# Performance work log

Measured on AMD Instinct MI355X. Metric: run time of the kernel, lower is better.

The kernel has to match this reference:

```python
import jax, jax.numpy as jnp
import numpy as np

K_TOP = 2
NUM_HEADS = 8
NOISE_EPS = 0.01
GATE_EPS = 1e-9
LOSS_COEF = 0.01


def _xavier(key, shape):
    fan_in, fan_out = shape[-2], shape[-1]
    lim = float(np.sqrt(6.0 / (fan_in + fan_out)))
    return jax.random.uniform(key, shape, jnp.float32, -lim, lim)


def setup_inputs():
    key = jax.random.key(0)
    ks = jax.random.split(key, 12)
    B, S, D, E = 32, 512, 512, 8
    return {
        "q": jax.random.normal(ks[0], (B, S, D), jnp.float32),
        "k": jax.random.normal(ks[1], (B, S, D), jnp.float32),
        "v": jax.random.normal(ks[2], (B, S, D), jnp.float32),
        "mask": jnp.ones((1, 1, S, S), jnp.int32),
        "w_gate": _xavier(ks[3], (D, E)),
        "w_noise": _xavier(ks[4], (D, E)),
        "Wq": _xavier(ks[5], (E, D, D)),
        "bq": jnp.zeros((E, D), jnp.float32),
        "Wk": _xavier(ks[6], (E, D, D)),
        "bk": jnp.zeros((E, D), jnp.float32),
        "Wv": _xavier(ks[7], (E, D, D)),
        "bv": jnp.zeros((E, D), jnp.float32),
        "Wo": _xavier(ks[8], (E, D, D)),
        "bo": jnp.zeros((E, D), jnp.float32),
    }


def _cv_squared(x):
    # torch .var() is unbiased (ddof=1)
    return jnp.var(x, ddof=1) / (jnp.mean(x) ** 2 + 1e-10)


def _moe_attention(q, k, v, mask, w_gate, w_noise, Wq, bq, Wk, bk, Wv, bv, Wo, bo):
    B, S, D = q.shape
    E = w_gate.shape[1]
    H = NUM_HEADS
    dh = D // H

    # x[x != x] = 0 (in-place nan scrub of q, used for gating AND as query)
    qc = jnp.where(jnp.isnan(q), jnp.zeros((), q.dtype), q)

    # noisy top-k gating; the python loop sum_i x[:,i,:] @ W == x.sum(1) @ W
    xs = qc.sum(axis=1)                                  # [B, D]
    clean_logits = xs @ w_gate                           # [B, E]
    raw_noise = xs @ w_noise
    noise_std = jax.nn.softplus(raw_noise) + NOISE_EPS   # train=True
    noise = jax.random.normal(jax.random.key(42), clean_logits.shape, clean_logits.dtype)
    noisy_logits = clean_logits + noise * noise_std

    top_logits, top_idx = jax.lax.top_k(noisy_logits, K_TOP + 1)  # [B, k+1]
    tk_logits = top_logits[:, :K_TOP]
    tk_idx = top_idx[:, :K_TOP]                          # [B, k]
    tk_gates = jax.nn.softmax(tk_logits, axis=1) + GATE_EPS
    gates = jnp.zeros((B, E), clean_logits.dtype).at[jnp.arange(B)[:, None], tk_idx].set(tk_gates)

    # load via prob-in-top-k (noisy_gating and k < num_experts)
    thr_in = top_logits[:, K_TOP][:, None]
    thr_out = top_logits[:, K_TOP - 1][:, None]
    is_in = noisy_logits > thr_in
    cdf = jax.scipy.stats.norm.cdf
    prob = jnp.where(is_in, cdf((clean_logits - thr_in) / noise_std),
                     cdf((clean_logits - thr_out) / noise_std))
    load = prob.sum(axis=0)
    importance = gates.sum(axis=0)
    loss = (_cv_squared(importance) + _cv_squared(load)) * LOSS_COEF

    # sparse dispatch == per (batch, slot) run the selected expert's MHA.
    # Gather expert weights per selected slot: [B, k, D, D].
    def proj(x, W, b):
        return jnp.einsum('bsd,bjdf->bjsf', x, W[tk_idx]) + b[tk_idx][:, :, None, :]

    Q = proj(qc, Wq, bq).reshape(B, K_TOP, S, H, dh)
    Kx = proj(k, Wk, bk).reshape(B, K_TOP, S, H, dh)
    V = proj(v, Wv, bv).reshape(B, K_TOP, S, H, dh)

    scale = jnp.asarray(1.0 / np.sqrt(dh), q.dtype)
    scores = jnp.einsum('bjqhd,bjkhd->bjhqk', Q, Kx) * scale   # [B,k,H,S,S]
    m = mask[:, None]                                          # [1,1,1,S,S]
    scores = jnp.where(m == 0, jnp.asarray(-1e9, scores.dtype), scores)
    attn = jax.nn.softmax(scores, axis=-1)
    ctx = jnp.einsum('bjhqk,bjkhd->bjqhd', attn, V).reshape(B, K_TOP, S, D)
    out_e = jnp.einsum('bjsd,bjdf->bjsf', ctx, Wo[tk_idx]) + bo[tk_idx][:, :, None, :]

    # combine: sum_j gate * exp(out), clamp zeros to eps, log
    combined = jnp.einsum('bj,bjsd->bsd', tk_gates, jnp.exp(out_e))
    eps = jnp.asarray(np.finfo(np.float64).eps, combined.dtype)
    combined = jnp.where(combined == 0, eps, combined)
    return jnp.log(combined), loss


def reference(q, k, v, mask, w_gate, w_noise, Wq, bq, Wk, bk, Wv, bv, Wo, bo):
    return _moe_attention(q, k, v, mask, w_gate, w_noise, Wq, bq, Wk, bk, Wv, bv, Wo, bo)
```

## Files before the change

### kernel.cpp

```cpp
#include <hip/hip_runtime.h>
#include <math.h>

typedef unsigned int u32;
typedef unsigned long long u64;
typedef unsigned short u16t;

#define SD   512
#define EE   8
#define DH   64
#define SDSQ (512*512)
#define LDSW 72

typedef __attribute__((ext_vector_type(8))) short bfrag8;
typedef __attribute__((ext_vector_type(4))) float f32x4;
typedef __attribute__((ext_vector_type(8))) unsigned short u16x8;

typedef const __attribute__((address_space(1))) void gas_void;
typedef __attribute__((address_space(3))) void las_void;

#define MFMA_B16(a,b,c) __builtin_amdgcn_mfma_f32_16x16x32_bf16((a),(b),(c),0,0,0)

__device__ __forceinline__ u32 rotl32(u32 x, int r){ return (x<<r)|(x>>(32-r)); }

__device__ __forceinline__ u16t bf_hi(float a){
  u32 x; __builtin_memcpy(&x,&a,4);
  u32 r = x + 0x7fffu + ((x>>16)&1u);
  return (u16t)(r>>16);
}
__device__ __forceinline__ float bf_f(u16t h){
  u32 x = ((u32)h)<<16; float f; __builtin_memcpy(&f,&x,4); return f;
}
__device__ __forceinline__ void split2(float a, u16t& h, u16t& l){
  h = bf_hi(a);
  l = bf_hi(a - bf_f(h));
}

__device__ __forceinline__ void gload16(const u16t* g, u16t* l){
  __builtin_amdgcn_global_load_lds((gas_void*)g, (las_void*)l, 16, 0, 0);
}

__device__ __forceinline__ void threefry_0_42(u32 x0, u32 x1, u32& o0, u32& o1){
  const u32 k0=0u, k1=42u;
  const u32 ks2 = k0 ^ k1 ^ 0x1BD11BDAu;
  const int R0[4]={13,15,26,6}, R1[4]={17,29,16,24};
  x0 += k0; x1 += k1;
  #pragma unroll
  for(int r=0;r<4;r++){ x0+=x1; x1=rotl32(x1,R0[r]); x1^=x0; }
  x0+=k1; x1+=ks2+1u;
  #pragma unroll
  for(int r=0;r<4;r++){ x0+=x1; x1=rotl32(x1,R1[r]); x1^=x0; }
  x0+=ks2; x1+=k0+2u;
  #pragma unroll
  for(int r=0;r<4;r++){ x0+=x1; x1=rotl32(x1,R0[r]); x1^=x0; }
  x0+=k0; x1+=k1+3u;
  #pragma unroll
  for(int r=0;r<4;r++){ x0+=x1; x1=rotl32(x1,R1[r]); x1^=x0; }
  x0+=k1; x1+=ks2+4u;
  #pragma unroll
  for(int r=0;r<4;r++){ x0+=x1; x1=rotl32(x1,R0[r]); x1^=x0; }
  x0+=ks2; x1+=k0+5u;
  o0 = x0; o1 = x1;
}

__device__ double erfinv64(double x){
  double w = -log((1.0 - x) * (1.0 + x));
  double p;
  if (w < 5.0){
    w = w - 2.5;
    p = 2.81022636e-08;
    p = 3.43273939e-07 + p*w;
    p = -3.5233877e-06 + p*w;
    p = -4.39150654e-06 + p*w;
    p = 0.00021858087  + p*w;
    p = -0.00125372503 + p*w;
    p = -0.00417768164 + p*w;
    p = 0.246640727    + p*w;
    p = 1.50140941     + p*w;
  } else {
    w = sqrt(w) - 3.0;
    p = -0.000200214257;
    p = 0.000100950558 + p*w;
    p = 0.00134934322  + p*w;
    p = -0.00367342844 + p*w;
    p = 0.00573950773  + p*w;
    p = -0.0076224613  + p*w;
    p = 0.00943887047  + p*w;
    p = 1.00167406     + p*w;
    p = 2.83297682     + p*w;
  }
  double r = p * x;
  #pragma unroll
  for (int it=0; it<2; ++it){
    double e = erf(r) - x;
    r -= e / (1.1283791670955126 * exp(-r*r));
  }
  return r;
}

__device__ double jax_noise_part32(int i){
  u32 o0, o1;
  threefry_0_42(0u, (u32)i, o0, o1);
  u32 bits = o0 ^ o1;
  u32 fb = (bits >> 9) | 0x3f800000u;
  float f; __builtin_memcpy(&f, &fb, 4);
  f -= 1.0f;
  u32 lob = 0xBF7FFFFFu;
  float lo; __builtin_memcpy(&lo, &lob, 4);
  float t = f * 2.0f;
  float u = t + lo;
  u = fmaxf(u, lo);
  return 1.4142135623730951 * erfinv64((double)u);
}

__global__ __launch_bounds__(256) void k_cvt_x(
  const float* __restrict__ src, u16t* __restrict__ dh, u16t* __restrict__ dl, int clean)
{
  const int n4 = 32*SDSQ/4;
  int i = blockIdx.x*256 + threadIdx.x;
  if (i >= n4) return;
  float4 r = ((const float4*)src)[i];
  float a[4] = {r.x, r.y, r.z, r.w};
  if (clean){
    #pragma unroll
    for (int u=0;u<4;u++) if (isnan(a[u])) a[u] = 0.f;
  }
  u16t h[4], l[4];
  #pragma unroll
  for (int u=0;u<4;u++) split2(a[u], h[u], l[u]);
  ((ushort4*)dh)[i] = make_ushort4(h[0],h[1],h[2],h[3]);
  ((ushort4*)dl)[i] = make_ushort4(l[0],l[1],l[2],l[3]);
}

__global__ __launch_bounds__(256) void k_cvt_w(
  const float* __restrict__ W, u16t* __restrict__ th, u16t* __restrict__ tl)
{
  __shared__ u16t Th[64*LDSW], Tl[64*LDSW];
  int e = blockIdx.z;
  int k0 = blockIdx.y*64, f0 = blockIdx.x*64;
  int tid = threadIdx.x;
  int r = tid>>2, c4 = (tid&3)*16;
  const float* Wp = W + (size_t)e*SDSQ + (size_t)(k0+r)*SD + f0 + c4;
  #pragma unroll
  for (int i=0;i<4;i++){
    float4 rv = *(const float4*)(Wp + 4*i);
    float a[4]={rv.x,rv.y,rv.z,rv.w};
    #pragma unroll
    for (int u=0;u<4;u++){
      u16t h,l; split2(a[u],h,l);
      Th[(c4+4*i+u)*LDSW + r] = h;
      Tl[(c4+4*i+u)*LDSW + r] = l;
    }
  }
  __syncthreads();
  u16t* dh = th + (size_t)e*SDSQ + (size_t)(f0+r)*SD + k0 + c4;
  u16t* dl = tl + (size_t)e*SDSQ + (size_t)(f0+r)*SD + k0 + c4;
  *(u16x8*)dh     = *(const u16x8*)&Th[r*LDSW + c4];
  *(u16x8*)(dh+8) = *(const u16x8*)&Th[r*LDSW + c4 + 8];
  *(u16x8*)dl     = *(const u16x8*)&Tl[r*LDSW + c4];
  *(u16x8*)(dl+8) = *(const u16x8*)&Tl[r*LDSW + c4 + 8];
}

__global__ void k_xs(const float* __restrict__ q, double* __restrict__ xs){
  int b = blockIdx.x, d = threadIdx.x;
  const float* p = q + (size_t)b*SDSQ + d;
  double acc = 0.0;
  for (int s=0; s<SD; ++s){
    float f = p[(size_t)s*SD];
    if (!isnan(f)) acc += (double)f;
  }
  xs[b*SD + d] = acc;
}

__global__ __launch_bounds__(256) void k_gate(
    const double* __restrict__ xs, const float* __restrict__ wg,
    const float* __restrict__ wn, int* __restrict__ tk_idx,
    float* __restrict__ tk_gates, float* __restrict__ out_loss)
{
  __shared__ double cl_s[256], sd_s[256], nz_s[256], pr_s[256];
  __shared__ double thrI_s[32], thrO_s[32], g0_s[32], g1_s[32];
  __shared__ int i0_s[32], i1_s[32];
  int tid = threadIdx.x;
  int b = tid >> 3, e = tid & 7;
  double c=0.0, n=0.0;
  const double* xr = xs + b*SD;
  for (int d=0; d<SD; ++d){
    double x = xr[d];
    c += x * (double)wg[d*EE + e];
    n += x * (double)wn[d*EE + e];
  }
  double sp = fmax(n, 0.0) + log1p(exp(-fabs(n)));
  double sdv = sp + 0.01;
  double nz = c + jax_noise_part32(tid) * sdv;
  cl_s[tid]=c; sd_s[tid]=sdv; nz_s[tid]=nz;
  __syncthreads();
  if (tid < 32){
    int bb = tid;
    double v0=-INFINITY,v1=-INFINITY,v2=-INFINITY; int i0=0,i1=0;
    for (int ee=0; ee<8; ++ee){
      double vv = nz_s[bb*8+ee];
      if (vv > v0){ v2=v1; v1=v0;i1=i0; v0=vv;i0=ee; }
      else if (vv > v1){ v2=v1; v1=vv;i1=ee; }
      else if (vv > v2){ v2=vv; }
    }
    double e1 = exp(v1 - v0);
    double s = 1.0 + e1;
    double g0 = 1.0/s + 1e-9, g1 = e1/s + 1e-9;
    tk_idx[bb*2+0]=i0; tk_idx[bb*2+1]=i1;
    tk_gates[bb*2+0]=(float)g0; tk_gates[bb*2+1]=(float)g1;
    i0_s[bb]=i0; i1_s[bb]=i1; g0_s[bb]=g0; g1_s[bb]=g1;
    thrI_s[bb]=v2; thrO_s[bb]=v1;
  }
  __syncthreads();
  {
    double thrI = thrI_s[b], thrO = thrO_s[b];
    bool isin = nz_s[tid] > thrI;
    double t = (cl_s[tid] - (isin ? thrI : thrO)) / sd_s[tid];
    pr_s[tid] = 0.5 * (1.0 + erf(t * 0.7071067811865476));
  }
  __syncthreads();
  if (tid == 0){
    double imp[8], ld[8];
    for (int i=0;i<8;i++){ imp[i]=0.0; ld[i]=0.0; }
    for (int bb=0; bb<32; ++bb){
      imp[i0_s[bb]] += g0_s[bb];
      imp[i1_s[bb]] += g1_s[bb];
    }
    for (int i=0;i<256;i++) ld[i&7] += pr_s[i];
    double loss = 0.0;
    for (int a=0;a<2;a++){
      double* arr = a ? ld : imp;
      double mu=0.0; for(int i=0;i<8;i++) mu += arr[i]; mu *= 0.125;
      double var=0.0; for(int i=0;i<8;i++){ double dd=arr[i]-mu; var += dd*dd; }
      var *= (1.0/7.0);
      loss += var / (mu*mu + 1e-10);
    }
    loss *= 0.01;
    out_loss[0] = (float)loss;
  }
}

__global__ __launch_bounds__(256) void k_proj(
  const u16t* __restrict__ qh, const u16t* __restrict__ ql,
  const u16t* __restrict__ kh, const u16t* __restrict__ kl,
  const u16t* __restrict__ vh, const u16t* __restrict__ vl,
  const u16t* __restrict__ wqh, const u16t* __restrict__ wql,
  const u16t* __restrict__ wkh, const u16t* __restrict__ wkl,
  const u16t* __restrict__ wvh, const u16t* __restrict__ wvl,
  const float* __restrict__ bq, const float* __restrict__ bk, const float* __restrict__ bv,
  const int* __restrict__ tk_idx, int pair0,
  u16t* __restrict__ Qh, u16t* __restrict__ Ql,
  u16t* __restrict__ Kh, u16t* __restrict__ Kl,
  u16t* __restrict__ Vth, u16t* __restrict__ Vtl)
{
  __shared__ __align__(16) u16t SM[4*128*64];
  int Nb = gridDim.x*gridDim.y*gridDim.z;
  int flat = blockIdx.x + gridDim.x*(blockIdx.y + gridDim.y*blockIdx.z);
  int nf = (flat & 7)*(Nb>>3) + (flat>>3);
  int bxx = nf & 3, byy = (nf>>2) & 3, z = nf >> 4;
  int lp = z/3, m = z - lp*3;
  int gp = pair0 + lp;
  int b = gp >> 1;
  int e = tk_idx[gp] & 7;
  const u16t *Xh, *Xl, *Wh, *Wl; const float* bias; u16t *Yh, *Yl;
  if (m==0){ Xh=qh; Xl=ql; Wh=wqh; Wl=wql; bias=bq; Yh=Qh;  Yl=Ql;  }
  else if (m==1){ Xh=kh; Xl=kl; Wh=wkh; Wl=wkl; bias=bk; Yh=Kh;  Yl=Kl;  }
  else { Xh=vh; Xl=vl; Wh=wvh; Wl=wvl; bias=bv; Yh=Vth; Yl=Vtl; }
  bool tr = (m==2);
  Xh += (size_t)b*SDSQ; Xl += (size_t)b*SDSQ;
  Wh += (size_t)e*SDSQ; Wl += (size_t)e*SDSQ;
  bias += e*SD;
  Yh += (size_t)lp*SDSQ; Yl += (size_t)lp*SDSQ;

  int tid = threadIdx.x, w = tid>>6, lane = tid&63;
  int q16 = lane&15, quad = lane>>4;
  int wm = w>>1, wnn = w&1;
  int s0 = byy*128, f0 = bxx*128;
  int row8 = lane>>3, cc = lane&7;
  int soff = (cc ^ row8)*8;
  int sw = q16 & 7;
  int aH_off = tr ? 16384 : 0;
  int bH_off = tr ? 0 : 16384;

  f32x4 acc[4][4];
  #pragma unroll
  for (int i=0;i<4;i++)
    #pragma unroll
    for (int j=0;j<4;j++) acc[i][j] = (f32x4){0.f,0.f,0.f,0.f};

  for (int k0=0;k0<SD;k0+=64){
    #pragma unroll
    for (int t=0;t<4;t++){
      int br = w*32 + t*8;
      int gr = br + row8;
      size_t ga  = (size_t)(s0+gr)*SD + k0 + soff;
      size_t gbo = (size_t)(f0+gr)*SD + k0 + soff;
      gload16(Xh + ga,  &SM[0     + br*64]);
      gload16(Xl + ga,  &SM[8192  + br*64]);
      gload16(Wh + gbo, &SM[16384 + br*64]);
      gload16(Wl + gbo, &SM[24576 + br*64]);
    }
    __syncthreads();
    #pragma unroll
    for (int kk=0;kk<2;kk++){
      int ch = kk*4 + quad;
      int co = (ch ^ sw)*8;
      bfrag8 fAH[4], fAL[4], fBH[4], fBL[4];
      #pragma unroll
      for (int i=0;i<4;i++){
        int ra = wm*64  + i*16 + q16;
        int rb = wnn*64 + i*16 + q16;
        fAH[i] = *(const bfrag8*)&SM[aH_off        + ra*64 + co];
        fAL[i] = *(const bfrag8*)&SM[aH_off + 8192 + ra*64 + co];
        fBH[i] = *(const bfrag8*)&SM[bH_off        + rb*64 + co];
        fBL[i] = *(const bfrag8*)&SM[bH_off + 8192 + rb*64 + co];
      }
      #pragma unroll
      for (int i=0;i<4;i++)
        #pragma unroll
        for (int j=0;j<4;j++){
          acc[i][j] = MFMA_B16(fAH[i], fBH[j], acc[i][j]);
          acc[i][j] = MFMA_B16(fAH[i], fBL[j], acc[i][j]);
          acc[i][j] = MFMA_B16(fAL[i], fBH[j], acc[i][j]);
        }
    }
    __syncthreads();
  }
  if (!tr){
    #pragma unroll
    for (int i=0;i<4;i++){
      #pragma unroll
      for (int j=0;j<4;j++){
        int f = f0 + wnn*64 + j*16 + q16;
        float bb = bias[f];
        #pragma unroll
        for (int rr=0;rr<4;rr++){
          int s = s0 + wm*64 + i*16 + quad*4 + rr;
          u16t hh, ll; split2(acc[i][j][rr] + bb, hh, ll);
          size_t o = (size_t)s*SD + f;
          Yh[o] = hh; Yl[o] = ll;
        }
      }
    }
  } else {
    #pragma unroll
    for (int i=0;i<4;i++){
      #pragma unroll
      for (int rr=0;rr<4;rr++){
        int fr = f0 + wm*64 + i*16 + quad*4 + rr;
        float bb = bias[fr];
        #pragma unroll
        for (int j=0;j<4;j++){
          int scol = s0 + wnn*64 + j*16 + q16;
          u16t hh, ll; split2(acc[i][j][rr] + bb, hh, ll);
          size_t o = (size_t)fr*SD + scol;
          Yh[o] = hh; Yl[o] = ll;
        }
      }
    }
  }
}

__global__ __launch_bounds__(256, 4) void k_attn(
  const u16t* __restrict__ Qh, const u16t* __restrict__ Ql,
  const u16t* __restrict__ Kh, const u16t* __restrict__ Kl,
  const u16t* __restrict__ Vth, const u16t* __restrict__ Vtl,
  u16t* __restrict__ Ch, u16t* __restrict__ Cl)
{
  __shared__ __align__(16) u16t SM[20480];
  int tid = threadIdx.x;
  int w = tid>>6, lane = tid&63, q16 = lane&15, quad = lane>>4;
  int Nb = gridDim.x*gridDim.y*gridDim.z;
  int flat = blockIdx.x + gridDim.x*(blockIdx.y + gridDim.y*blockIdx.z);
  int nf = (flat & 7)*(Nb>>3) + (flat>>3);
  int qt = nf & 7, h = (nf>>3) & 7, lp = nf >> 6;
  int s0 = qt*64;
  const size_t base  = (size_t)lp*SDSQ + h*DH;
  const size_t vbase = (size_t)lp*SDSQ + (size_t)h*DH*SD;
  int row8 = lane>>3, cc = lane&7;
  int soff = (cc ^ row8)*8;
  int sw = q16 & 7;

  bfrag8 qH[2], qL[2];
  {
    const u16t* qp  = Qh + base + (size_t)(s0 + w*16 + q16)*SD + quad*8;
    const u16t* qp2 = Ql + base + (size_t)(s0 + w*16 + q16)*SD + quad*8;
    qH[0] = *(const bfrag8*)(qp);
    qH[1] = *(const bfrag8*)(qp + 32);
    qL[0] = *(const bfrag8*)(qp2);
    qL[1] = *(const bfrag8*)(qp2 + 32);
  }

  float m_row[4], l_row[4];
  f32x4 ctx[4];
  #pragma unroll
  for (int rr=0;rr<4;rr++){ m_row[rr]=-INFINITY; l_row[rr]=0.f; }
  #pragma unroll
  for (int nt=0;nt<4;nt++) ctx[nt] = (f32x4){0.f,0.f,0.f,0.f};

  for (int kt=0; kt<8; ++kt){
    #pragma unroll
    for (int t=0;t<2;t++){
      int br = w*16 + t*8;
      int gr = br + row8;
      size_t gk = base + (size_t)(kt*64+gr)*SD + soff;
      gload16(Kh + gk, &SM[0    + br*64]);
      gload16(Kl + gk, &SM[4096 + br*64]);
      size_t gv = vbase + (size_t)gr*SD + kt*64 + soff;
      gload16(Vth + gv, &SM[8192  + br*64]);
      gload16(Vtl + gv, &SM[12288 + br*64]);
    }
    __syncthreads();

    f32x4 sc[4];
    #pragma unroll
    for (int nt=0;nt<4;nt++) sc[nt] = (f32x4){0.f,0.f,0.f,0.f};
    #pragma unroll
    for (int kk=0;kk<2;kk++){
      int co = ((kk*4+quad) ^ sw)*8;
      #pragma unroll
      for (int nt=0;nt<4;nt++){
        bfrag8 bH = *(const bfrag8*)&SM[0    + (nt*16+q16)*64 + co];
        bfrag8 bL = *(const bfrag8*)&SM[4096 + (nt*16+q16)*64 + co];
        sc[nt] = MFMA_B16(qH[kk],bH,sc[nt]);
        sc[nt] = MFMA_B16(qH[kk],bL,sc[nt]);
        sc[nt] = MFMA_B16(qL[kk],bH,sc[nt]);
      }
    }
    #pragma unroll
    for (int nt=0;nt<4;nt++)
      #pragma unroll
      for (int rr=0;rr<4;rr++) sc[nt][rr] *= 0.125f;

    float alpha[4];
    #pragma unroll
    for (int rr=0;rr<4;rr++){
      float mx = sc[0][rr];
      #pragma unroll
      for (int nt=1;nt<4;nt++) mx = fmaxf(mx, sc[nt][rr]);
      mx = fmaxf(mx, __shfl_xor(mx, 1));
      mx = fmaxf(mx, __shfl_xor(mx, 2));
      mx = fmaxf(mx, __shfl_xor(mx, 4));
      mx = fmaxf(mx, __shfl_xor(mx, 8));
      float nm = fmaxf(m_row[rr], mx);
      alpha[rr] = expf(m_row[rr] - nm);
      m_row[rr] = nm;
    }
    #pragma unroll
    for (int rr=0;rr<4;rr++){
      float S = 0.f;
      #pragma unroll
      for (int nt=0;nt<4;nt++){
        float p = expf(sc[nt][rr] - m_row[rr]);
        sc[nt][rr] = p;
        S += p;
      }
      S += __shfl_xor(S, 1);
      S += __shfl_xor(S, 2);
      S += __shfl_xor(S, 4);
      S += __shfl_xor(S, 8);
      l_row[rr] = l_row[rr]*alpha[rr] + S;
      #pragma unroll
      for (int nt=0;nt<4;nt++) ctx[nt][rr] *= alpha[rr];
    }
    #pragma unroll
    for (int nt=0;nt<4;nt++){
      int c = nt*2 + (q16>>3);
      #pragma unroll
      for (int rr=0;rr<4;rr++){
        int prow = quad*4 + rr;
        SM[16384 + (w*16+prow)*64 + ((c ^ (prow&7))*8) + (q16&7)] = bf_hi(sc[nt][rr]);
      }
    }

    #pragma unroll
    for (int kk2=0;kk2<2;kk2++){
      int co2 = ((kk2*4+quad) ^ sw)*8;
      bfrag8 aP = *(const bfrag8*)&SM[16384 + (w*16+q16)*64 + co2];
      #pragma unroll
      for (int nt=0;nt<4;nt++){
        bfrag8 vH = *(const bfrag8*)&SM[8192  + (nt*16+q16)*64 + co2];
        bfrag8 vL = *(const bfrag8*)&SM[12288 + (nt*16+q16)*64 + co2];
        ctx[nt] = MFMA_B16(aP,vH,ctx[nt]);
        ctx[nt] = MFMA_B16(aP,vL,ctx[nt]);
      }
    }
    __syncthreads();
  }
  #pragma unroll
  for (int rr=0;rr<4;rr++){
    float inv = 1.f / l_row[rr];
    #pragma unroll
    for (int nt=0;nt<4;nt++){
      int s = s0 + w*16 + quad*4 + rr;
      u16t hh, ll; split2(ctx[nt][rr]*inv, hh, ll);
      size_t o = base + (size_t)s*SD + nt*16 + q16;
      Ch[o] = hh; Cl[o] = ll;
    }
  }
}

__global__ __launch_bounds__(256) void k_out(
  const u16t* __restrict__ Ch, const u16t* __restrict__ Cl,
  const u16t* __restrict__ Wth, const u16t* __restrict__ Wtl,
  const float* __restrict__ bo, const int* __restrict__ tk_idx,
  const float* __restrict__ tk_gates, int pair0, float* __restrict__ out)
{
  __shared__ __align__(16) u16t Ah[64*64], Al[64*64];
  __shared__ __align__(16) u16t Bh[64*64], Bl[64*64];
  int Nb = gridDim.x*gridDim.y*gridDim.z;
  int flat = blockIdx.x + gridDim.x*(blockIdx.y + gridDim.y*blockIdx.z);
  int nf = (flat & 7)*(Nb>>3) + (flat>>3);
  int bxx = nf & 7, byy = (nf>>3) & 7, lb = nf >> 6;
  int gb = (pair0 >> 1) + lb;
  int tid = threadIdx.x;
  int w = tid>>6, lane = tid&63, q16 = lane&15, quad = lane>>4;
  int s0 = byy*64, f0 = bxx*64;
  int row8 = lane>>3, cc = lane&7;
  int soff = (cc ^ row8)*8;
  int sw = q16 & 7;

  f32x4 acc2[2][4];
  #pragma unroll
  for (int j=0;j<2;j++)
    #pragma unroll
    for (int nt=0;nt<4;nt++) acc2[j][nt] = (f32x4){0.f,0.f,0.f,0.f};

  for (int j=0;j<2;++j){
    int e = tk_idx[pair0 + lb*2 + j] & 7;
    const u16t* AH = Ch + (size_t)(lb*2+j)*SDSQ;
    const u16t* AL = Cl + (size_t)(lb*2+j)*SDSQ;
    const u16t* WH = Wth + (size_t)e*SDSQ;
    const u16t* WL = Wtl + (size_t)e*SDSQ;
    for (int k0=0;k0<SD;k0+=64){
      #pragma unroll
      for (int t=0;t<2;t++){
        int br = w*16 + t*8, gr = br + row8;
        size_t ga  = (size_t)(s0+gr)*SD + k0 + soff;
        size_t gbo = (size_t)(f0+gr)*SD + k0 + soff;
        gload16(AH + ga,  &Ah[br*64]);
        gload16(AL + ga,  &Al[br*64]);
        gload16(WH + gbo, &Bh[br*64]);
        gload16(WL + gbo, &Bl[br*64]);
      }
      __syncthreads();
      #pragma unroll
      for (int kk=0;kk<2;kk++){
        int co = ((kk*4+quad) ^ sw)*8;
        bfrag8 aH = *(const bfrag8*)&Ah[(w*16+q16)*64 + co];
        bfrag8 aL = *(const bfrag8*)&Al[(w*16+q16)*64 + co];
        #pragma unroll
        for (int nt=0;nt<4;nt++){
          bfrag8 bH = *(const bfrag8*)&Bh[(nt*16+q16)*64 + co];
          bfrag8 bL = *(const bfrag8*)&Bl[(nt*16+q16)*64 + co];
          acc2[j][nt] = MFMA_B16(aH,bH,acc2[j][nt]);
          acc2[j][nt] = MFMA_B16(aH,bL,acc2[j][nt]);
          acc2[j][nt] = MFMA_B16(aL,bH,acc2[j][nt]);
        }
      }
      __syncthreads();
    }
  }
  int e0 = tk_idx[pair0 + lb*2 + 0] & 7, e1 = tk_idx[pair0 + lb*2 + 1] & 7;
  float g0 = tk_gates[pair0 + lb*2 + 0], g1 = tk_gates[pair0 + lb*2 + 1];
  #pragma unroll
  for (int nt=0;nt<4;nt++){
    #pragma unroll
    for (int rr=0;rr<4;rr++){
      int s = s0 + w*16 + quad*4 + rr;
      int f = f0 + nt*16 + q16;
      float o0 = acc2[0][nt][rr] + bo[e0*SD+f];
      float o1 = acc2[1][nt][rr] + bo[e1*SD+f];
      float cmb = g0*expf(o0) + g1*expf(o1);
      if (cmb == 0.f) cmb = 2.2204460492503131e-16f;
      out[(size_t)gb*SDSQ + (size_t)s*SD + f] = logf(cmb);
    }
  }
}

extern "C" void kernel_launch(void* const* d_in, const int* in_sizes, int n_in,
                              void* d_out, int out_size, void* d_ws, size_t ws_size,
                              hipStream_t stream)
{
  const float* q  = (const float*)d_in[0];
  const float* k  = (const float*)d_in[1];
  const float* v  = (const float*)d_in[2];
  const float* wg = (const float*)d_in[4];
  const float* wn = (const float*)d_in[5];
  const float* Wq = (const float*)d_in[6];
  const float* bq = (const float*)d_in[7];
  const float* Wk = (const float*)d_in[8];
  const float* bk = (const float*)d_in[9];
  const float* Wv = (const float*)d_in[10];
  const float* bv = (const float*)d_in[11];
  const float* Wo = (const float*)d_in[12];
  const float* bo = (const float*)d_in[13];
  float* out = (float*)d_out;

  char* ws = (char*)d_ws;
  double* xs      = (double*)(ws + 0);
  int*   tk_idx   = (int*)  (ws + 131072);
  float* tk_gates = (float*)(ws + 131072 + 256);

  const size_t header = (size_t)1 << 20;
  const size_t XSB = (size_t)32 * SDSQ * 2;
  const size_t WSB = (size_t)8  * SDSQ * 2;
  u16t* qch = (u16t*)(ws + header + 0*XSB);
  u16t* qcl = (u16t*)(ws + header + 1*XSB);
  u16t* kh_ = (u16t*)(ws + header + 2*XSB);
  u16t* kl_ = (u16t*)(ws + header + 3*XSB);
  u16t* vh_ = (u16t*)(ws + header + 4*XSB);
  u16t* vl_ = (u16t*)(ws + header + 5*XSB);
  char* wbase = ws + header + 6*XSB;
  u16t* wqh = (u16t*)(wbase + 0*WSB);
  u16t* wql = (u16t*)(wbase + 1*WSB);
  u16t* wkh = (u16t*)(wbase + 2*WSB);
  u16t* wkl = (u16t*)(wbase + 3*WSB);
  u16t* wvh = (u16t*)(wbase + 4*WSB);
  u16t* wvl = (u16t*)(wbase + 5*WSB);
  u16t* woh = (u16t*)(wbase + 6*WSB);
  u16t* wol = (u16t*)(wbase + 7*WSB);
  char* bufbase = wbase + 8*WSB;

  const size_t slab = (size_t)SDSQ * 2;
  size_t used = (size_t)(bufbase - ws);
  size_t avail = (ws_size > used) ? (ws_size - used) : 0;
  int CH = (int)(avail / (6 * slab));
  CH &= ~1;
  if (CH > 64) CH = 64;
  if (CH < 2)  CH = 2;

  k_cvt_x<<<dim3(8192), dim3(256), 0, stream>>>(q, qch, qcl, 1);
  k_cvt_x<<<dim3(8192), dim3(256), 0, stream>>>(k, kh_, kl_, 0);
  k_cvt_x<<<dim3(8192), dim3(256), 0, stream>>>(v, vh_, vl_, 0);
  k_cvt_w<<<dim3(8,8,8), dim3(256), 0, stream>>>(Wq, wqh, wql);
  k_cvt_w<<<dim3(8,8,8), dim3(256), 0, stream>>>(Wk, wkh, wkl);
  k_cvt_w<<<dim3(8,8,8), dim3(256), 0, stream>>>(Wv, wvh, wvl);
  k_cvt_w<<<dim3(8,8,8), dim3(256), 0, stream>>>(Wo, woh, wol);

  k_xs  <<<dim3(32), dim3(512), 0, stream>>>(q, xs);
  k_gate<<<dim3(1), dim3(256), 0, stream>>>(xs, wg, wn, tk_idx, tk_gates,
                                            out + (size_t)out_size - 1);

  for (int pair0 = 0; pair0 < 64; pair0 += CH){
    int cur = (64 - pair0 < CH) ? (64 - pair0) : CH;
    u16t* Qh  = (u16t*)bufbase;
    u16t* Ql  = Qh  + (size_t)CH * SDSQ;
    u16t* Kh  = Ql  + (size_t)CH * SDSQ;
    u16t* Kl  = Kh  + (size_t)CH * SDSQ;
    u16t* Vth = Kl  + (size_t)CH * SDSQ;
    u16t* Vtl = Vth + (size_t)CH * SDSQ;
    u16t* Ch = Qh;
    u16t* Cl = Ql;

    k_proj<<<dim3(4,4,cur*3), dim3(256), 0, stream>>>(
        qch,qcl, kh_,kl_, vh_,vl_, wqh,wql, wkh,wkl, wvh,wvl,
        bq,bk,bv, tk_idx, pair0, Qh,Ql, Kh,Kl, Vth,Vtl);
    k_attn<<<dim3(8,8,cur), dim3(256), 0, stream>>>(Qh,Ql, Kh,Kl, Vth,Vtl, Ch,Cl);
    k_out <<<dim3(8,8,cur/2), dim3(256), 0, stream>>>(Ch,Cl, woh,wol, bo, tk_idx, tk_gates,
                                                      pair0, out);
  }
}
```

Measured before the change: 761.7 us.

## Fold softmax scale into Q projection, use exp2 and lazy rescaling in attention

Folds the 1/sqrt(dh)*log2(e) factor into the Q projection output so the attention kernel can use exp2f directly with no per-score multiply. The online softmax now rescales the running max, sum and context only when some row's max has grown by more than 8 (in log2 units), checked wave-wide with __any. The final combine uses exp2/log2, and the column-sum kernel is relaunched with more, smaller blocks. The lazy rescale allows unnormalised probabilities up to 2^8, which may cost some bf16 precision in P.

```diff
diff --git a/kernel.cpp b/kernel.cpp
--- a/kernel.cpp
+++ b/kernel.cpp
@@ -10,6 +10,10 @@
 #define DH   64
 #define SDSQ (512*512)
 #define LDSW 72
+
+#define QSC  0.18033688011112042f
+#define LOG2E 1.4426950408889634f
+#define LN2   0.6931471805599453f
 
 typedef __attribute__((ext_vector_type(8))) short bfrag8;
 typedef __attribute__((ext_vector_type(4))) float f32x4;
@@ -161,7 +165,7 @@
 }
 
 __global__ void k_xs(const float* __restrict__ q, double* __restrict__ xs){
-  int b = blockIdx.x, d = threadIdx.x;
+  int b = blockIdx.x, d = blockIdx.y*128 + threadIdx.x;
   const float* p = q + (size_t)b*SDSQ + d;
   double acc = 0.0;
   for (int s=0; s<SD; ++s){
@@ -266,6 +270,7 @@
   else if (m==1){ Xh=kh; Xl=kl; Wh=wkh; Wl=wkl; bias=bk; Yh=Kh;  Yl=Kl;  }
   else { Xh=vh; Xl=vl; Wh=wvh; Wl=wvl; bias=bv; Yh=Vth; Yl=Vtl; }
   bool tr = (m==2);
+  float ysc = (m==0) ? QSC : 1.0f;
   Xh += (size_t)b*SDSQ; Xl += (size_t)b*SDSQ;
   Wh += (size_t)e*SDSQ; Wl += (size_t)e*SDSQ;
   bias += e*SD;
@@ -335,7 +340,7 @@
         #pragma unroll
         for (int rr=0;rr<4;rr++){
           int s = s0 + wm*64 + i*16 + quad*4 + rr;
-          u16t hh, ll; split2(acc[i][j][rr] + bb, hh, ll);
+          u16t hh, ll; split2((acc[i][j][rr] + bb)*ysc, hh, ll);
           size_t o = (size_t)s*SD + f;
           Yh[o] = hh; Yl[o] = ll;
         }
@@ -426,12 +431,9 @@
         sc[nt] = MFMA_B16(qL[kk],bH,sc[nt]);
       }
     }
-    #pragma unroll
-    for (int nt=0;nt<4;nt++)
-      #pragma unroll
-      for (int rr=0;rr<4;rr++) sc[nt][rr] *= 0.125f;
-
-    float alpha[4];
+
+    float mx4[4];
+    bool grow = false;
     #pragma unroll
     for (int rr=0;rr<4;rr++){
       float mx = sc[0][rr];
@@ -441,16 +443,26 @@
       mx = fmaxf(mx, __shfl_xor(mx, 2));
       mx = fmaxf(mx, __shfl_xor(mx, 4));
       mx = fmaxf(mx, __shfl_xor(mx, 8));
-      float nm = fmaxf(m_row[rr], mx);
-      alpha[rr] = expf(m_row[rr] - nm);
-      m_row[rr] = nm;
+      mx4[rr] = mx;
+      grow = grow || (mx > m_row[rr] + 8.f);
+    }
+    if (__any(grow ? 1 : 0)){
+      #pragma unroll
+      for (int rr=0;rr<4;rr++){
+        float nm = fmaxf(m_row[rr], mx4[rr]);
+        float al = exp2f(m_row[rr] - nm);
+        m_row[rr] = nm;
+        l_row[rr] *= al;
+        #pragma unroll
+        for (int nt=0;nt<4;nt++) ctx[nt][rr] *= al;
+      }
     }
     #pragma unroll
     for (int rr=0;rr<4;rr++){
       float S = 0.f;
       #pragma unroll
       for (int nt=0;nt<4;nt++){
-        float p = expf(sc[nt][rr] - m_row[rr]);
+        float p = exp2f(sc[nt][rr] - m_row[rr]);
         sc[nt][rr] = p;
         S += p;
       }
@@ -458,9 +470,7 @@
       S += __shfl_xor(S, 2);
       S += __shfl_xor(S, 4);
       S += __shfl_xor(S, 8);
-      l_row[rr] = l_row[rr]*alpha[rr] + S;
-      #pragma unroll
-      for (int nt=0;nt<4;nt++) ctx[nt][rr] *= alpha[rr];
+      l_row[rr] += S;
     }
     #pragma unroll
     for (int nt=0;nt<4;nt++){
@@ -570,9 +580,9 @@
       int f = f0 + nt*16 + q16;
       float o0 = acc2[0][nt][rr] + bo[e0*SD+f];
       float o1 = acc2[1][nt][rr] + bo[e1*SD+f];
-      float cmb = g0*expf(o0) + g1*expf(o1);
+      float cmb = g0*exp2f(o0*LOG2E) + g1*exp2f(o1*LOG2E);
       if (cmb == 0.f) cmb = 2.2204460492503131e-16f;
-      out[(size_t)gb*SDSQ + (size_t)s*SD + f] = logf(cmb);
+      out[(size_t)gb*SDSQ + (size_t)s*SD + f] = log2f(cmb)*LN2;
     }
   }
 }
@@ -637,7 +647,7 @@
   k_cvt_w<<<dim3(8,8,8), dim3(256), 0, stream>>>(Wv, wvh, wvl);
   k_cvt_w<<<dim3(8,8,8), dim3(256), 0, stream>>>(Wo, woh, wol);
 
-  k_xs  <<<dim3(32), dim3(512), 0, stream>>>(q, xs);
+  k_xs  <<<dim3(32,4), dim3(128), 0, stream>>>(q, xs);
   k_gate<<<dim3(1), dim3(256), 0, stream>>>(xs, wg, wn, tk_idx, tk_gates,
                                             out + (size_t)out_size - 1);
 
```

New measurement: 697.2 us. -8.5%, faster.
